# Optimization experiments

Measured on AMD Instinct MI355X. Metric: run time of the kernel, lower is better.

## Reference

```python
import jax, jax.numpy as jnp
import numpy as np

EMBED = 1536
HEADS = 12
EPS = 1e-5


def _layernorm(x, gamma, beta):
    mu = x.mean(axis=-1, keepdims=True)
    var = ((x - mu) ** 2).mean(axis=-1, keepdims=True)
    return (x - mu) * jax.lax.rsqrt(var + EPS) * gamma + beta


def setup_inputs() -> dict:
    key = jax.random.key(0)
    ks = jax.random.split(key, 8)
    N, L, E = 8, 2048, EMBED
    x = jax.random.normal(ks[0], (N, L, E), dtype=jnp.float32)
    s = 0.02
    Wv = jax.random.normal(ks[1], (E, E), dtype=jnp.float32) * s
    Wk = jax.random.normal(ks[2], (E, E), dtype=jnp.float32) * s
    Wq = jax.random.normal(ks[3], (E, E), dtype=jnp.float32) * s
    Wo = jax.random.normal(ks[4], (E, E), dtype=jnp.float32) * s
    bo = jnp.zeros((E,), dtype=jnp.float32)
    gamma = jnp.ones((E,), dtype=jnp.float32)
    beta = jnp.zeros((E,), dtype=jnp.float32)
    return {"combined_embeddings": x, "Wv": Wv, "Wk": Wk, "Wq": Wq,
            "Wo": Wo, "bo": bo, "gamma": gamma, "beta": beta}


def reference(combined_embeddings, Wv, Wk, Wq, Wo, bo, gamma, beta):
    x = combined_embeddings
    N, L, E = x.shape
    H, hd = HEADS, E // HEADS
    # projections (torch Linear: x @ W^T), reshape to (N, H, L, hd)
    v = (x @ Wv.T).reshape(N, L, H, hd).transpose(0, 2, 1, 3)
    k = (x @ Wk.T).reshape(N, L, H, hd).transpose(0, 2, 1, 3)
    q = (x @ Wq.T).reshape(N, L, H, hd).transpose(0, 2, 1, 3)
    # NOTE: faithful to the source, einsum labels treat axis1 (heads) as q/k
    # and axis2 (sequence) as h -> heads-over-heads attention per position.
    energy = jnp.einsum('nqhd,nkhd->nhqk', q, k)  # (N, L, H, H)
    attention = jax.nn.softmax(energy / jnp.sqrt(jnp.float32(E)), axis=3)
    out = jnp.einsum('nhql,nlhd->nqhd', attention, v)  # (N, H, L, hd)
    out = out.transpose(0, 2, 1, 3).reshape(N, L, E)
    out = out @ Wo.T + bo
    out = _layernorm(out + x, gamma, beta)
    # small extra attention
    e_actions = out[:, 2:][None]          # (1, N, L-2, E)
    e_state = out.mean(axis=1)[None]      # (1, N, E)
    scores = jnp.matmul(e_state, jnp.swapaxes(e_actions, -2, -1))
    scores = scores / jnp.sqrt(jnp.float32(E))   # (1, N, N, L-2)
    weights = jax.nn.softmax(scores, axis=-1)
    attended = jnp.matmul(weights, e_actions)    # (1, N, N, E)
    return attended, weights
```

## Files before the change

kernel.cpp:

```cpp
#include <hip/hip_runtime.h>
#include <stdint.h>

typedef unsigned short u16;
typedef __bf16 bf16_t;
typedef bf16_t bf16x8 __attribute__((ext_vector_type(8)));
typedef float f32x4 __attribute__((ext_vector_type(4)));

#define E_DIM 1536
#define N_B 8
#define L_SEQ 2048
#define NT 2046
#define SCALE 0.025515518f
#define LN_EPS 1e-5f
#define NTILES 24

__device__ __forceinline__ u16 f2b(float f) {
  union { float f; uint32_t u; } v; v.f = f;
  uint32_t u = v.u + 0x7FFFu + ((v.u >> 16) & 1u);
  return (u16)(u >> 16);
}
__device__ __forceinline__ float b2f(u16 h) {
  union { uint32_t u; float f; } v; v.u = ((uint32_t)h) << 16; return v.f;
}

__device__ __forceinline__ void gload16(const u16* g, const bf16_t* l) {
  __builtin_amdgcn_global_load_lds((const __attribute__((address_space(1))) void*)g,
                                   (__attribute__((address_space(3))) void*)l,
                                   16, 0, 0);
}

#define BAR()   __builtin_amdgcn_s_barrier()
#define SCHB()  __builtin_amdgcn_sched_barrier(0)
#define VM4()   asm volatile("s_waitcnt vmcnt(4)" ::: "memory")
#define VM0()   asm volatile("s_waitcnt vmcnt(0)" ::: "memory")

__global__ void cvt_kernel(const float* __restrict__ in, u16* __restrict__ out, int nvec) {
  int i = blockIdx.x * 256 + threadIdx.x;
  if (i < nvec) {
    float4 f = ((const float4*)in)[i];
    ushort4 u;
    u.x = f2b(f.x); u.y = f2b(f.y); u.z = f2b(f.z); u.w = f2b(f.w);
    ((ushort4*)out)[i] = u;
  }
}

template<int FUSED>
__launch_bounds__(512, 2)
__global__ void gemm2c(const u16* __restrict__ Ag,
                       const u16* __restrict__ B0w, const u16* __restrict__ B1w,
                       const u16* __restrict__ B2w,
                       u16* __restrict__ C0, u16* __restrict__ C1, u16* __restrict__ C2,
                       float* __restrict__ Cf, const float* __restrict__ bias,
                       const float* __restrict__ resid)
{
  extern __shared__ __attribute__((aligned(16))) bf16_t lds[];

  const int flat = (blockIdx.z * gridDim.y + blockIdx.y) * gridDim.x + blockIdx.x;
  const int xcd = flat & 7, bb_ = flat >> 3;
  const int gl = bb_ / 24, jj = bb_ % 24;
  const int g = gl * 8 + xcd;
  const int zz = g >> 4;
  const int gy = g & 15;
  const int tx = jj >> 2;
  const int ty = gy * 4 + (jj & 3);
  const int rowA = ty * 256, colB = tx * 256;

  const u16* Bg; u16* Cb;
  if (zz == 0)      { Bg = B0w; Cb = C0; }
  else if (zz == 1) { Bg = B1w; Cb = C1; }
  else              { Bg = B2w; Cb = C2; }

  const int tid = threadIdx.x;
  const int w = tid >> 6, lane = tid & 63;
  const int wr = w >> 2, wc = w & 3;

  const int rl = lane & 15, lsl = lane >> 4;
  const int sw8 = (lsl ^ ((rl >> 1) & 3)) * 8;
  const int arow = (wr * 128 + rl) * 32 + sw8;
  const int brow = (wc * 64 + rl) * 32 + sw8;

  const int r0s = tid >> 2, sps = tid & 3;
  const int sws = (sps ^ ((r0s >> 1) & 3)) * 8;
  const size_t sA0 = (size_t)(rowA + r0s) * E_DIM + sws;
  const size_t sA1 = (size_t)(rowA + 128 + r0s) * E_DIM + sws;
  const size_t sB0 = (size_t)(colB + r0s) * E_DIM + sws;
  const size_t sB1 = (size_t)(colB + 128 + r0s) * E_DIM + sws;
  const int wb0 = w * 512, wb1 = 4096 + w * 512;

  f32x4 acc[8][4];
#pragma unroll
  for (int m = 0; m < 8; ++m)
#pragma unroll
    for (int n = 0; n < 4; ++n)
#pragma unroll
      for (int q = 0; q < 4; ++q) acc[m][n][q] = 0.0f;

  gload16(Ag + sA0,      lds + 0     + wb0);  gload16(Ag + sA1,      lds + 0     + wb1);
  gload16(Bg + sB0,      lds + 32768 + wb0);  gload16(Bg + sB1,      lds + 32768 + wb1);
  gload16(Ag + sA0 + 32, lds + 8192  + wb0);  gload16(Ag + sA1 + 32, lds + 8192  + wb1);
  gload16(Bg + sB0 + 32, lds + 40960 + wb0);  gload16(Bg + sB1 + 32, lds + 40960 + wb1);
  gload16(Ag + sA0 + 64, lds + 16384 + wb0);  gload16(Ag + sA1 + 64, lds + 16384 + wb1);
  gload16(Bg + sB0 + 64, lds + 49152 + wb0);  gload16(Bg + sB1 + 64, lds + 49152 + wb1);
  VM4();
  BAR();

  bf16x8 a0[8], b0[4], a1[8], b1[4];
#pragma unroll
  for (int m = 0; m < 8; ++m) a0[m] = *(const bf16x8*)&lds[0 + arow + m * 512];
#pragma unroll
  for (int n = 0; n < 4; ++n) b0[n] = *(const bf16x8*)&lds[32768 + brow + n * 512];

  for (int t = 0; t < NTILES; ++t) {
    const int cur = t & 1, nxt = cur ^ 1;
    const int Ak1 = (cur * 2 + 1) * 8192, Bk1 = 32768 + (cur * 2 + 1) * 8192;
    const int AkN0 = nxt * 2 * 8192,      BkN0 = 32768 + nxt * 2 * 8192;
    const int AkN1 = (nxt * 2 + 1) * 8192, BkN1 = 32768 + (nxt * 2 + 1) * 8192;

#pragma unroll
    for (int m = 0; m < 8; ++m) a1[m] = *(const bf16x8*)&lds[Ak1 + arow + m * 512];
#pragma unroll
    for (int n = 0; n < 4; ++n) b1[n] = *(const bf16x8*)&lds[Bk1 + brow + n * 512];
    if (t + 1 < NTILES) {
      const size_t ko = (size_t)(t + 1) * 64 + 32;
      gload16(Ag + sA0 + ko, lds + AkN1 + wb0);  gload16(Ag + sA1 + ko, lds + AkN1 + wb1);
      gload16(Bg + sB0 + ko, lds + BkN1 + wb0);  gload16(Bg + sB1 + ko, lds + BkN1 + wb1);
    }
    SCHB();
    __builtin_amdgcn_s_setprio(1);
#pragma unroll
    for (int m = 0; m < 8; ++m)
#pragma unroll
      for (int n = 0; n < 4; ++n)
        acc[m][n] = __builtin_amdgcn_mfma_f32_16x16x32_bf16(a0[m], b0[n], acc[m][n], 0, 0, 0);
    __builtin_amdgcn_s_setprio(0);
    SCHB();
    if (t + 1 < NTILES) { VM4(); }
    BAR();

    if (t + 2 < NTILES) {
      const size_t ko = (size_t)(t + 2) * 64;
      gload16(Ag + sA0 + ko, lds + cur * 2 * 8192 + wb0);
      gload16(Ag + sA1 + ko, lds + cur * 2 * 8192 + wb1);
      gload16(Bg + sB0 + ko, lds + 32768 + cur * 2 * 8192 + wb0);
      gload16(Bg + sB1 + ko, lds + 32768 + cur * 2 * 8192 + wb1);
    }
    if (t + 1 < NTILES) {
#pragma unroll
      for (int m = 0; m < 8; ++m) a0[m] = *(const bf16x8*)&lds[AkN0 + arow + m * 512];
#pragma unroll
      for (int n = 0; n < 4; ++n) b0[n] = *(const bf16x8*)&lds[BkN0 + brow + n * 512];
    }
    SCHB();
    __builtin_amdgcn_s_setprio(1);
#pragma unroll
    for (int m = 0; m < 8; ++m)
#pragma unroll
      for (int n = 0; n < 4; ++n)
        acc[m][n] = __builtin_amdgcn_mfma_f32_16x16x32_bf16(a1[m], b1[n], acc[m][n], 0, 0, 0);
    __builtin_amdgcn_s_setprio(0);
    SCHB();
    if (t + 2 < NTILES)      { VM4(); }
    else if (t + 1 < NTILES) { VM0(); }
    BAR();
  }

  const int r0 = (lane >> 4) * 4;
#pragma unroll
  for (int m = 0; m < 8; ++m) {
#pragma unroll
    for (int n = 0; n < 4; ++n) {
      const int gcol = colB + wc * 64 + n * 16 + rl;
#pragma unroll
      for (int q = 0; q < 4; ++q) {
        const int grow = rowA + wr * 128 + m * 16 + r0 + q;
        const size_t idx = (size_t)grow * E_DIM + gcol;
        if (FUSED) Cf[idx] = acc[m][n][q] + bias[gcol] + resid[idx];
        else       Cb[idx] = f2b(acc[m][n][q]);
      }
    }
  }
}

__launch_bounds__(256)
__global__ void headmix(const u16* __restrict__ qb, const u16* __restrict__ kb,
                        const u16* __restrict__ vb, u16* __restrict__ aob)
{
  __shared__ float qs[12 * 132], ks2[12 * 132], vs[12 * 132];
  __shared__ float att[12][12];
  const int tid = threadIdx.x;
  const size_t base = (size_t)blockIdx.x * E_DIM;

  for (int e = tid; e < E_DIM; e += 256) {
    int i = e >> 7, d = e & 127, p = i * 132 + d;
    qs[p]  = b2f(qb[base + e]);
    ks2[p] = b2f(kb[base + e]);
    vs[p]  = b2f(vb[base + e]);
  }
  __syncthreads();

  if (tid < 144) {
    int i = tid / 12, j = tid % 12;
    float s = 0.f;
#pragma unroll 8
    for (int d = 0; d < 128; ++d) s += qs[i * 132 + d] * ks2[j * 132 + d];
    att[i][j] = s * SCALE;
  }
  __syncthreads();

  if (tid < 12) {
    float mx = att[tid][0];
#pragma unroll
    for (int j = 1; j < 12; ++j) mx = fmaxf(mx, att[tid][j]);
    float ev[12], sum = 0.f;
#pragma unroll
    for (int j = 0; j < 12; ++j) { ev[j] = expf(att[tid][j] - mx); sum += ev[j]; }
    float inv = 1.f / sum;
#pragma unroll
    for (int j = 0; j < 12; ++j) att[tid][j] = ev[j] * inv;
  }
  __syncthreads();

  for (int e = tid; e < E_DIM; e += 256) {
    int i = e >> 7, d = e & 127;
    float o = 0.f;
#pragma unroll
    for (int j = 0; j < 12; ++j) o += att[i][j] * vs[j * 132 + d];
    aob[base + e] = f2b(o);
  }
}

__launch_bounds__(256)
__global__ void ln_kernel(const float* __restrict__ p, u16* __restrict__ ho,
                          const float* __restrict__ gamma, const float* __restrict__ beta)
{
  __shared__ float rs[4], rq[4];
  __shared__ float mean_s, rstd_s;
  const int tid = threadIdx.x, w = tid >> 6, lane = tid & 63;
  const float* row = p + (size_t)blockIdx.x * E_DIM;
  u16* orow = ho + (size_t)blockIdx.x * E_DIM;

  float v[6], s = 0.f, sq = 0.f;
#pragma unroll
  for (int i = 0; i < 6; ++i) {
    v[i] = row[tid + i * 256];
    s += v[i]; sq += v[i] * v[i];
  }
#pragma unroll
  for (int off = 32; off > 0; off >>= 1) {
    s  += __shfl_down(s, off);
    sq += __shfl_down(sq, off);
  }
  if (lane == 0) { rs[w] = s; rq[w] = sq; }
  __syncthreads();
  if (tid == 0) {
    float S = rs[0] + rs[1] + rs[2] + rs[3];
    float Q = rq[0] + rq[1] + rq[2] + rq[3];
    float mu = S * (1.f / 1536.f);
    float var = Q * (1.f / 1536.f) - mu * mu;
    mean_s = mu; rstd_s = rsqrtf(var + LN_EPS);
  }
  __syncthreads();
  const float mu = mean_s, rstd = rstd_s;
#pragma unroll
  for (int i = 0; i < 6; ++i) {
    int e = tid + i * 256;
    orow[e] = f2b((v[i] - mu) * rstd * gamma[e] + beta[e]);
  }
}

__global__ void estate_partial(const u16* __restrict__ outp, float* __restrict__ part)
{
  const int e = blockIdx.x * 256 + threadIdx.x;
  const int b = blockIdx.y, z = blockIdx.z;
  const u16* p = outp + ((size_t)b * L_SEQ + z * 256) * E_DIM + e;
  float acc = 0.f;
  for (int l = 0; l < 256; ++l) acc += b2f(p[(size_t)l * E_DIM]);
  part[(size_t)(z * N_B + b) * E_DIM + e] = acc;
}
__global__ void estate_reduce(const float* __restrict__ part, float* __restrict__ est)
{
  const int i = blockIdx.x * 256 + threadIdx.x;
  if (i < N_B * E_DIM) {
    float s = 0.f;
#pragma unroll
    for (int z = 0; z < 8; ++z) s += part[(size_t)z * N_B * E_DIM + i];
    est[i] = s * (1.f / 2048.f);
  }
}

__launch_bounds__(256)
__global__ void scores_kernel(const u16* __restrict__ outp, const float* __restrict__ est,
                              float* __restrict__ wout)
{
  __shared__ float es[N_B * E_DIM];
  const int tid = threadIdx.x, wv = tid >> 6, lane = tid & 63;
  const int b = blockIdx.y;
  for (int i = tid; i < N_B * E_DIM; i += 256) es[i] = est[i];
  __syncthreads();

  for (int ti = 0; ti < 16; ++ti) {
    int t = blockIdx.x * 64 + wv * 16 + ti;
    if (t >= NT) continue;
    const uint32_t* row =
        (const uint32_t*)(outp + ((size_t)b * L_SEQ + 2 + t) * E_DIM);
    float a[8];
#pragma unroll
    for (int s = 0; s < 8; ++s) a[s] = 0.f;
    for (int c = 0; c < 12; ++c) {
      uint32_t pv = row[c * 64 + lane];
      float v0 = b2f((u16)(pv & 0xFFFF)), v1 = b2f((u16)(pv >> 16));
      int idx = (c * 64 + lane) * 2;
#pragma unroll
      for (int s = 0; s < 8; ++s)
        a[s] += es[s * E_DIM + idx] * v0 + es[s * E_DIM + idx + 1] * v1;
    }
#pragma unroll
    for (int off = 32; off > 0; off >>= 1)
#pragma unroll
      for (int s = 0; s < 8; ++s) a[s] += __shfl_down(a[s], off);
    if (lane == 0) {
#pragma unroll
      for (int s = 0; s < 8; ++s)
        wout[(size_t)(b * N_B + s) * NT + t] = a[s] * SCALE;
    }
  }
}

__launch_bounds__(256)
__global__ void softmax_w(float* __restrict__ wbase)
{
  float* p = wbase + (size_t)blockIdx.x * NT;
  __shared__ float r1[4], r2[4];
  __shared__ float bmax, bsum;
  const int tid = threadIdx.x, wv = tid >> 6, lane = tid & 63;

  float vals[8], mx = -1e30f;
#pragma unroll
  for (int i = 0; i < 8; ++i) {
    int t = tid + i * 256;
    vals[i] = (t < NT) ? p[t] : -1e30f;
    mx = fmaxf(mx, vals[i]);
  }
#pragma unroll
  for (int off = 32; off > 0; off >>= 1) mx = fmaxf(mx, __shfl_down(mx, off));
  if (lane == 0) r1[wv] = mx;
  __syncthreads();
  if (tid == 0) bmax = fmaxf(fmaxf(r1[0], r1[1]), fmaxf(r1[2], r1[3]));
  __syncthreads();
  mx = bmax;

  float sum = 0.f;
#pragma unroll
  for (int i = 0; i < 8; ++i) {
    int t = tid + i * 256;
    if (t < NT) { vals[i] = expf(vals[i] - mx); sum += vals[i]; }
  }
#pragma unroll
  for (int off = 32; off > 0; off >>= 1) sum += __shfl_down(sum, off);
  if (lane == 0) r2[wv] = sum;
  __syncthreads();
  if (tid == 0) bsum = r2[0] + r2[1] + r2[2] + r2[3];
  __syncthreads();
  const float inv = 1.f / bsum;
#pragma unroll
  for (int i = 0; i < 8; ++i) {
    int t = tid + i * 256;
    if (t < NT) p[t] = vals[i] * inv;
  }
}

__launch_bounds__(256)
__global__ void attended_partial(const u16* __restrict__ outp, const float* __restrict__ wts,
                                 float* __restrict__ part)
{
  const int tid = threadIdx.x;
  const int e = blockIdx.x * 256 + tid;
  const int b = blockIdx.y, z = blockIdx.z;
  __shared__ float wl[8][256];
  float a[8];
#pragma unroll
  for (int s = 0; s < 8; ++s) a[s] = 0.f;

  const int tbeg = z * 512;
  const int tend = (tbeg + 512 < NT) ? tbeg + 512 : NT;
  for (int tb = tbeg; tb < tend; tb += 256) {
    const int cnt = (tend - tb < 256) ? (tend - tb) : 256;
    __syncthreads();
    for (int i = tid; i < 8 * 256; i += 256) {
      int s = i >> 8, tt = i & 255;
      wl[s][tt] = (tt < cnt) ? wts[(size_t)(b * N_B + s) * NT + tb + tt] : 0.f;
    }
    __syncthreads();
    for (int tt = 0; tt < cnt; ++tt) {
      float val = b2f(outp[((size_t)b * L_SEQ + 2 + tb + tt) * E_DIM + e]);
#pragma unroll
      for (int s = 0; s < 8; ++s) a[s] += wl[s][tt] * val;
    }
  }
#pragma unroll
  for (int s = 0; s < 8; ++s)
    part[(((size_t)z * N_B + b) * N_B + s) * E_DIM + e] = a[s];
}
__global__ void attended_reduce(const float* __restrict__ part, float* __restrict__ outp)
{
  const int i = blockIdx.x * 256 + threadIdx.x;
  float s = 0.f;
#pragma unroll
  for (int z = 0; z < 4; ++z) s += part[(size_t)z * N_B * N_B * E_DIM + i];
  outp[i] = s;
}

extern "C" void kernel_launch(void* const* d_in, const int* in_sizes, int n_in,
                              void* d_out, int out_size, void* d_ws, size_t ws_size,
                              hipStream_t stream)
{
  (void)in_sizes; (void)n_in; (void)out_size; (void)ws_size;
  const float* x     = (const float*)d_in[0];
  const float* Wv    = (const float*)d_in[1];
  const float* Wk    = (const float*)d_in[2];
  const float* Wq    = (const float*)d_in[3];
  const float* Wo    = (const float*)d_in[4];
  const float* bo    = (const float*)d_in[5];
  const float* gamma = (const float*)d_in[6];
  const float* beta  = (const float*)d_in[7];
  float* out = (float*)d_out;

  char* ws = (char*)d_ws;
  size_t off = 0;
  auto alloc = [&](size_t bytes) -> void* {
    void* p = ws + off;
    off += (bytes + 255) & ~(size_t)255;
    return p;
  };
  const size_t ME = (size_t)16384 * E_DIM;
  const size_t WE = (size_t)E_DIM * E_DIM;
  u16*   xb    = (u16*)alloc(ME * 2);
  u16*   wqb   = (u16*)alloc(WE * 2);
  u16*   wkb   = (u16*)alloc(WE * 2);
  u16*   wvb   = (u16*)alloc(WE * 2);
  u16*   wob   = (u16*)alloc(WE * 2);
  u16*   qb    = (u16*)alloc(ME * 2);
  u16*   kb    = (u16*)alloc(ME * 2);
  u16*   vb    = (u16*)alloc(ME * 2);
  u16*   aob   = (u16*)alloc(ME * 2);
  float* lnbuf = (float*)alloc(ME * 4);
  float* est   = (float*)alloc((size_t)N_B * E_DIM * 4);
  float* estp  = (float*)alloc((size_t)8 * N_B * E_DIM * 4);
  float* attp  = (float*)alloc((size_t)4 * N_B * N_B * E_DIM * 4);

  float* wout = out + 98304;

  hipFuncSetAttribute(reinterpret_cast<const void*>(gemm2c<0>),
                      hipFuncAttributeMaxDynamicSharedMemorySize, 131072);
  hipFuncSetAttribute(reinterpret_cast<const void*>(gemm2c<1>),
                      hipFuncAttributeMaxDynamicSharedMemorySize, 131072);

  cvt_kernel<<<dim3((6291456 + 255) / 256), 256, 0, stream>>>(x, xb, 6291456);
  cvt_kernel<<<dim3((589824 + 255) / 256), 256, 0, stream>>>(Wq, wqb, 589824);
  cvt_kernel<<<dim3((589824 + 255) / 256), 256, 0, stream>>>(Wk, wkb, 589824);
  cvt_kernel<<<dim3((589824 + 255) / 256), 256, 0, stream>>>(Wv, wvb, 589824);
  cvt_kernel<<<dim3((589824 + 255) / 256), 256, 0, stream>>>(Wo, wob, 589824);

  gemm2c<0><<<dim3(6, 64, 3), 512, 131072, stream>>>(
      xb, wqb, wkb, wvb, qb, kb, vb, nullptr, nullptr, nullptr);

  headmix<<<dim3(16384), 256, 0, stream>>>(qb, kb, vb, aob);

  gemm2c<1><<<dim3(6, 64, 1), 512, 131072, stream>>>(
      aob, wob, wob, wob, nullptr, nullptr, nullptr, lnbuf, bo, x);

  u16* lnh = aob;
  ln_kernel<<<dim3(16384), 256, 0, stream>>>(lnbuf, lnh, gamma, beta);

  estate_partial<<<dim3(6, 8, 8), 256, 0, stream>>>(lnh, estp);
  estate_reduce<<<dim3(48), 256, 0, stream>>>(estp, est);

  scores_kernel<<<dim3(32, 8), 256, 0, stream>>>(lnh, est, wout);
  softmax_w<<<dim3(64), 256, 0, stream>>>(wout);

  attended_partial<<<dim3(6, 8, 4), 256, 0, stream>>>(lnh, wout, attp);
  attended_reduce<<<dim3(384), 256, 0, stream>>>(attp, out);
}
```

Baseline: 560.0 us.

## Store pre-LayerNorm activations in bf16, merge conversions, vectorize headmix and LN loads

The output-projection GEMM epilogue now writes bf16 instead of fp32 and reads the residual from the bf16 copy of x rather than the fp32 input. LayerNorm reads that bf16 buffer with packed 32-bit loads and stores. The five conversion launches are merged into one kernel, and headmix loads Q/K/V with 16-byte vectors and uses float4 dot products. The aim is to cut HBM traffic on the large intermediate and reduce launch count, at the cost of extra bf16 rounding on the residual and pre-norm values.

Measured after the change: 528.5 us. 5.6% less time.

```diff
diff --git a/kernel.cpp b/kernel.cpp
--- a/kernel.cpp
+++ b/kernel.cpp
@@ -13,6 +13,8 @@
 #define SCALE 0.025515518f
 #define LN_EPS 1e-5f
 #define NTILES 24
+#define NXV 6291456
+#define NWV 589824
 
 __device__ __forceinline__ u16 f2b(float f) {
   union { float f; uint32_t u; } v; v.f = f;
@@ -34,14 +36,24 @@
 #define VM4()   asm volatile("s_waitcnt vmcnt(4)" ::: "memory")
 #define VM0()   asm volatile("s_waitcnt vmcnt(0)" ::: "memory")
 
-__global__ void cvt_kernel(const float* __restrict__ in, u16* __restrict__ out, int nvec) {
+__global__ void cvt_all(const float* __restrict__ x,  const float* __restrict__ Wq,
+                        const float* __restrict__ Wk, const float* __restrict__ Wv,
+                        const float* __restrict__ Wo,
+                        u16* __restrict__ xb,  u16* __restrict__ wqb,
+                        u16* __restrict__ wkb, u16* __restrict__ wvb,
+                        u16* __restrict__ wob)
+{
   int i = blockIdx.x * 256 + threadIdx.x;
-  if (i < nvec) {
-    float4 f = ((const float4*)in)[i];
-    ushort4 u;
-    u.x = f2b(f.x); u.y = f2b(f.y); u.z = f2b(f.z); u.w = f2b(f.w);
-    ((ushort4*)out)[i] = u;
-  }
+  const float* src; u16* dst; int o;
+  if (i < NXV)              { src = x;  dst = xb;  o = i; }
+  else if (i < NXV + NWV)   { src = Wq; dst = wqb; o = i - NXV; }
+  else if (i < NXV + 2*NWV) { src = Wk; dst = wkb; o = i - NXV - NWV; }
+  else if (i < NXV + 3*NWV) { src = Wv; dst = wvb; o = i - NXV - 2*NWV; }
+  else                      { src = Wo; dst = wob; o = i - NXV - 3*NWV; }
+  float4 f = ((const float4*)src)[o];
+  ushort4 u;
+  u.x = f2b(f.x); u.y = f2b(f.y); u.z = f2b(f.z); u.w = f2b(f.w);
+  ((ushort4*)dst)[o] = u;
 }
 
 template<int FUSED>
@@ -50,8 +62,7 @@
                        const u16* __restrict__ B0w, const u16* __restrict__ B1w,
                        const u16* __restrict__ B2w,
                        u16* __restrict__ C0, u16* __restrict__ C1, u16* __restrict__ C2,
-                       float* __restrict__ Cf, const float* __restrict__ bias,
-                       const float* __restrict__ resid)
+                       const float* __restrict__ bias, const u16* __restrict__ resid16)
 {
   extern __shared__ __attribute__((aligned(16))) bf16_t lds[];
 
@@ -174,8 +185,10 @@
       for (int q = 0; q < 4; ++q) {
         const int grow = rowA + wr * 128 + m * 16 + r0 + q;
         const size_t idx = (size_t)grow * E_DIM + gcol;
-        if (FUSED) Cf[idx] = acc[m][n][q] + bias[gcol] + resid[idx];
-        else       Cb[idx] = f2b(acc[m][n][q]);
+        if (FUSED == 2)
+          Cb[idx] = f2b(acc[m][n][q] + bias[gcol] + b2f(resid16[idx]));
+        else
+          Cb[idx] = f2b(acc[m][n][q]);
       }
     }
   }
@@ -190,19 +203,34 @@
   const int tid = threadIdx.x;
   const size_t base = (size_t)blockIdx.x * E_DIM;
 
-  for (int e = tid; e < E_DIM; e += 256) {
-    int i = e >> 7, d = e & 127, p = i * 132 + d;
-    qs[p]  = b2f(qb[base + e]);
-    ks2[p] = b2f(kb[base + e]);
-    vs[p]  = b2f(vb[base + e]);
+  if (tid < 192) {
+    const int i = tid >> 4, d0 = (tid & 15) * 8, p = i * 132 + d0;
+    uint4 q4 = *(const uint4*)(qb + base + tid * 8);
+    uint4 k4 = *(const uint4*)(kb + base + tid * 8);
+    uint4 v4 = *(const uint4*)(vb + base + tid * 8);
+#pragma unroll
+    for (int c = 0; c < 4; ++c) {
+      uint32_t qa = (&q4.x)[c], ka = (&k4.x)[c], va = (&v4.x)[c];
+      qs[p + 2*c]     = b2f((u16)(qa & 0xFFFF));
+      qs[p + 2*c + 1] = b2f((u16)(qa >> 16));
+      ks2[p + 2*c]     = b2f((u16)(ka & 0xFFFF));
+      ks2[p + 2*c + 1] = b2f((u16)(ka >> 16));
+      vs[p + 2*c]     = b2f((u16)(va & 0xFFFF));
+      vs[p + 2*c + 1] = b2f((u16)(va >> 16));
+    }
   }
   __syncthreads();
 
   if (tid < 144) {
     int i = tid / 12, j = tid % 12;
+    const float4* qr = (const float4*)&qs[i * 132];
+    const float4* kr = (const float4*)&ks2[j * 132];
     float s = 0.f;
 #pragma unroll 8
-    for (int d = 0; d < 128; ++d) s += qs[i * 132 + d] * ks2[j * 132 + d];
+    for (int d4 = 0; d4 < 32; ++d4) {
+      float4 a = qr[d4], b = kr[d4];
+      s += a.x * b.x + a.y * b.y + a.z * b.z + a.w * b.w;
+    }
     att[i][j] = s * SCALE;
   }
   __syncthreads();
@@ -230,20 +258,22 @@
 }
 
 __launch_bounds__(256)
-__global__ void ln_kernel(const float* __restrict__ p, u16* __restrict__ ho,
+__global__ void ln_kernel(const u16* __restrict__ p, u16* __restrict__ ho,
                           const float* __restrict__ gamma, const float* __restrict__ beta)
 {
   __shared__ float rs[4], rq[4];
   __shared__ float mean_s, rstd_s;
   const int tid = threadIdx.x, w = tid >> 6, lane = tid & 63;
-  const float* row = p + (size_t)blockIdx.x * E_DIM;
-  u16* orow = ho + (size_t)blockIdx.x * E_DIM;
+  const uint32_t* row = (const uint32_t*)(p + (size_t)blockIdx.x * E_DIM);
+  uint32_t* orow = (uint32_t*)(ho + (size_t)blockIdx.x * E_DIM);
 
   float v[6], s = 0.f, sq = 0.f;
 #pragma unroll
-  for (int i = 0; i < 6; ++i) {
-    v[i] = row[tid + i * 256];
-    s += v[i]; sq += v[i] * v[i];
+  for (int i = 0; i < 3; ++i) {
+    uint32_t u = row[tid + i * 256];
+    float lo = b2f((u16)(u & 0xFFFF)), hi = b2f((u16)(u >> 16));
+    v[2*i] = lo; v[2*i+1] = hi;
+    s += lo + hi; sq += lo * lo + hi * hi;
   }
 #pragma unroll
   for (int off = 32; off > 0; off >>= 1) {
@@ -262,9 +292,11 @@
   __syncthreads();
   const float mu = mean_s, rstd = rstd_s;
 #pragma unroll
-  for (int i = 0; i < 6; ++i) {
-    int e = tid + i * 256;
-    orow[e] = f2b((v[i] - mu) * rstd * gamma[e] + beta[e]);
+  for (int i = 0; i < 3; ++i) {
+    int j = tid + i * 256;
+    float o0 = (v[2*i]   - mu) * rstd * gamma[2*j]   + beta[2*j];
+    float o1 = (v[2*i+1] - mu) * rstd * gamma[2*j+1] + beta[2*j+1];
+    orow[j] = (uint32_t)f2b(o0) | ((uint32_t)f2b(o1) << 16);
   }
 }
 
@@ -434,43 +466,40 @@
   };
   const size_t ME = (size_t)16384 * E_DIM;
   const size_t WE = (size_t)E_DIM * E_DIM;
-  u16*   xb    = (u16*)alloc(ME * 2);
-  u16*   wqb   = (u16*)alloc(WE * 2);
-  u16*   wkb   = (u16*)alloc(WE * 2);
-  u16*   wvb   = (u16*)alloc(WE * 2);
-  u16*   wob   = (u16*)alloc(WE * 2);
-  u16*   qb    = (u16*)alloc(ME * 2);
-  u16*   kb    = (u16*)alloc(ME * 2);
-  u16*   vb    = (u16*)alloc(ME * 2);
-  u16*   aob   = (u16*)alloc(ME * 2);
-  float* lnbuf = (float*)alloc(ME * 4);
-  float* est   = (float*)alloc((size_t)N_B * E_DIM * 4);
-  float* estp  = (float*)alloc((size_t)8 * N_B * E_DIM * 4);
-  float* attp  = (float*)alloc((size_t)4 * N_B * N_B * E_DIM * 4);
+  u16*   xb     = (u16*)alloc(ME * 2);
+  u16*   wqb    = (u16*)alloc(WE * 2);
+  u16*   wkb    = (u16*)alloc(WE * 2);
+  u16*   wvb    = (u16*)alloc(WE * 2);
+  u16*   wob    = (u16*)alloc(WE * 2);
+  u16*   qb     = (u16*)alloc(ME * 2);
+  u16*   kb     = (u16*)alloc(ME * 2);
+  u16*   vb     = (u16*)alloc(ME * 2);
+  u16*   aob    = (u16*)alloc(ME * 2);
+  u16*   lnbufh = (u16*)alloc(ME * 2);
+  float* est    = (float*)alloc((size_t)N_B * E_DIM * 4);
+  float* estp   = (float*)alloc((size_t)8 * N_B * E_DIM * 4);
+  float* attp   = (float*)alloc((size_t)4 * N_B * N_B * E_DIM * 4);
 
   float* wout = out + 98304;
 
   hipFuncSetAttribute(reinterpret_cast<const void*>(gemm2c<0>),
                       hipFuncAttributeMaxDynamicSharedMemorySize, 131072);
-  hipFuncSetAttribute(reinterpret_cast<const void*>(gemm2c<1>),
+  hipFuncSetAttribute(reinterpret_cast<const void*>(gemm2c<2>),
                       hipFuncAttributeMaxDynamicSharedMemorySize, 131072);
 
-  cvt_kernel<<<dim3((6291456 + 255) / 256), 256, 0, stream>>>(x, xb, 6291456);
-  cvt_kernel<<<dim3((589824 + 255) / 256), 256, 0, stream>>>(Wq, wqb, 589824);
-  cvt_kernel<<<dim3((589824 + 255) / 256), 256, 0, stream>>>(Wk, wkb, 589824);
-  cvt_kernel<<<dim3((589824 + 255) / 256), 256, 0, stream>>>(Wv, wvb, 589824);
-  cvt_kernel<<<dim3((589824 + 255) / 256), 256, 0, stream>>>(Wo, wob, 589824);
+  cvt_all<<<dim3((NXV + 4 * NWV) / 256), 256, 0, stream>>>(
+      x, Wq, Wk, Wv, Wo, xb, wqb, wkb, wvb, wob);
 
   gemm2c<0><<<dim3(6, 64, 3), 512, 131072, stream>>>(
-      xb, wqb, wkb, wvb, qb, kb, vb, nullptr, nullptr, nullptr);
+      xb, wqb, wkb, wvb, qb, kb, vb, nullptr, nullptr);
 
   headmix<<<dim3(16384), 256, 0, stream>>>(qb, kb, vb, aob);
 
-  gemm2c<1><<<dim3(6, 64, 1), 512, 131072, stream>>>(
-      aob, wob, wob, wob, nullptr, nullptr, nullptr, lnbuf, bo, x);
+  gemm2c<2><<<dim3(6, 64, 1), 512, 131072, stream>>>(
+      aob, wob, wob, wob, lnbufh, lnbufh, lnbufh, bo, xb);
 
   u16* lnh = aob;
-  ln_kernel<<<dim3(16384), 256, 0, stream>>>(lnbuf, lnh, gamma, beta);
+  ln_kernel<<<dim3(16384), 256, 0, stream>>>(lnbufh, lnh, gamma, beta);
 
   estate_partial<<<dim3(6, 8, 8), 256, 0, stream>>>(lnh, estp);
   estate_reduce<<<dim3(48), 256, 0, stream>>>(estp, est);
```
